# Performance work log

Measured on AMD Instinct MI355X. Metric: run time of the kernel, lower is better.

The kernel has to match this reference:

```python
import jax, jax.numpy as jnp
import numpy as np

B, T, D, H = 2, 2048, 1024, 16
DH = D // H  # 64


def setup_inputs() -> dict:
    key = jax.random.key(0)
    k1, k2, k3 = jax.random.split(key, 3)
    x = jax.random.normal(k1, (B, T, D), dtype=jnp.float32)
    # torch nn.Linear(d, 3d, bias=False): y = x @ W.T; we store W already transposed as [in, out]
    Wqkv = jax.random.normal(k2, (D, 3 * D), dtype=jnp.float32) * (1.0 / np.sqrt(D))
    Wproj = jax.random.normal(k3, (D, D), dtype=jnp.float32) * (1.0 / np.sqrt(D))
    return {"x": x, "Wqkv": Wqkv, "Wproj": Wproj}


def reference(x, Wqkv, Wproj):
    Bx, Tx, C = x.shape
    qkv = x @ Wqkv                                   # [B,T,3C]
    q, k, v = jnp.split(qkv, 3, axis=-1)
    def rs(t):
        return t.reshape(Bx, Tx, H, DH).transpose(0, 2, 1, 3)  # [B,H,T,DH]
    q, k, v = rs(q), rs(k), rs(v)
    scale = 1.0 / jnp.sqrt(jnp.asarray(DH, dtype=x.dtype))
    att = jnp.einsum('bhqd,bhkd->bhqk', q, k) * scale          # [B,H,T,T]
    causal = jnp.tril(jnp.ones((Tx, Tx), dtype=bool))
    att = jnp.where(causal[None, None, :, :], att, jnp.asarray(-jnp.inf, dtype=att.dtype))
    att = jax.nn.softmax(att, axis=-1)
    out = jnp.einsum('bhqk,bhkd->bhqd', att, v)                # [B,H,T,DH]
    out = out.transpose(0, 2, 1, 3).reshape(Bx, Tx, C)         # [B,T,C]
    return out @ Wproj
```

## Files before the change

kernel.cpp:

```cpp
#include <hip/hip_runtime.h>
#include <hip/hip_bf16.h>

#define BB 2
#define TT 2048
#define DD 1024
#define HH 16
#define MM (BB*TT)
#define N3 (3*DD)
#define QKW 2048

typedef __attribute__((ext_vector_type(8))) short short8;
typedef __attribute__((ext_vector_type(4))) float f32x4;
typedef __attribute__((ext_vector_type(16))) float f32x16;

#define ZERO16 (f32x16){0,0,0,0,0,0,0,0,0,0,0,0,0,0,0,0}

#define GLDS16(g, l) __builtin_amdgcn_global_load_lds( \
    (const __attribute__((address_space(1))) void*)(g), \
    (__attribute__((address_space(3))) void*)(l), 16, 0, 0)

__device__ __forceinline__ unsigned short f2bf(float f) {
    union { float f; unsigned u; } v; v.f = f;
    unsigned r = v.u + 0x7FFFu + ((v.u >> 16) & 1u);
    return (unsigned short)(r >> 16);
}

__device__ __forceinline__ unsigned cvt_pk_bf16(float lo, float hi) {
    unsigned r;
    asm("v_cvt_pk_bf16_f32 %0, %1, %2" : "=v"(r) : "v"(lo), "v"(hi));
    return r;
}

__device__ __forceinline__ float fast_exp2(float x) {
    float r;
    asm("v_exp_f32 %0, %1" : "=v"(r) : "v"(x));
    return r;
}
__device__ __forceinline__ float fast_rcp(float x) {
    float r;
    asm("v_rcp_f32 %0, %1" : "=v"(r) : "v"(x));
    return r;
}

__global__ void prep_kernel(const float* __restrict__ x,
                            const float* __restrict__ Wqkv,
                            const float* __restrict__ Wproj,
                            unsigned short* __restrict__ xb,
                            unsigned short* __restrict__ wqkvt,
                            unsigned short* __restrict__ wprojt) {
    __shared__ float tile[32][33];
    const int bid = blockIdx.x;
    const int tx = threadIdx.x, ty = threadIdx.y;
    if (bid < 4096) {
        const float* src;
        unsigned short* dst;
        int rows, cols, c0, r0;
        if (bid < 3072) {
            src = Wqkv; dst = wqkvt; rows = DD; cols = N3;
            c0 = (bid % 96) * 32; r0 = (bid / 96) * 32;
        } else {
            src = Wproj; dst = wprojt; rows = DD; cols = DD;
            int b2 = bid - 3072;
            c0 = (b2 & 31) * 32; r0 = (b2 >> 5) * 32;
        }
#pragma unroll
        for (int i = 0; i < 4; i++) {
            int r = ty + i * 8;
            tile[r][tx] = src[(size_t)(r0 + r) * cols + c0 + tx];
        }
        __syncthreads();
#pragma unroll
        for (int i = 0; i < 4; i++) {
            int r = ty + i * 8;
            dst[(size_t)(c0 + r) * rows + r0 + tx] = f2bf(tile[tx][r]);
        }
    } else {
        const int t = ty * 32 + tx;
        int i = (bid - 4096) * 256 + t;
#pragma unroll
        for (int k = 0; k < 2; k++, i += 262144) {
            const float4* s = reinterpret_cast<const float4*>(x) + (size_t)i * 2;
            float4 a = s[0], b = s[1];
            unsigned short r[8] = {f2bf(a.x), f2bf(a.y), f2bf(a.z), f2bf(a.w),
                                   f2bf(b.x), f2bf(b.y), f2bf(b.z), f2bf(b.w)};
            *reinterpret_cast<uint4*>(xb + (size_t)i * 8) = *reinterpret_cast<uint4*>(r);
        }
    }
}

__global__ __launch_bounds__(512, 2)
void gemm256_qkv(const unsigned short* __restrict__ A,
                 const unsigned short* __restrict__ Bt,
                 unsigned short* __restrict__ qkv2,
                 unsigned short* __restrict__ Vout,
                 float scale) {
    __shared__ unsigned short Al[2][2][128][64];
    __shared__ unsigned short Bl[2][2][128][64];

    const int id = blockIdx.y * 12 + blockIdx.x;
    const int swzid = (id & 7) * 24 + (id >> 3);
    const int tm = (swzid / 12) * 256, tn = (swzid % 12) * 256;
    const int t = threadIdx.x, w = t >> 6, l = t & 63;
    const int wm = w >> 2, wn = w & 3, bh = wn >> 1;
    const int lo = l & 15, hi = l >> 4;
    const int srow = l >> 3;
    const int sg = (l & 7) ^ srow;

    f32x4 acc[8][4];
#pragma unroll
    for (int i = 0; i < 8; i++)
#pragma unroll
        for (int j = 0; j < 4; j++) acc[i][j] = (f32x4){0.f, 0.f, 0.f, 0.f};

    const unsigned short* Abase = A + (size_t)(tm + w * 16 + srow) * 1024 + sg * 8;
    const unsigned short* Bbase = Bt + (size_t)(tn + w * 16 + srow) * 1024 + sg * 8;

#define STG_A(KT, H) { \
    GLDS16(Abase + (size_t)(H) * 128 * 1024 + ((KT) & 15) * 64, &Al[(KT) & 1][H][w * 16][0]); \
    GLDS16(Abase + (size_t)(H) * 128 * 1024 + 8 * 1024 + ((KT) & 15) * 64, &Al[(KT) & 1][H][w * 16 + 8][0]); }
#define STG_B(KT, H) { \
    GLDS16(Bbase + (size_t)(H) * 128 * 1024 + ((KT) & 15) * 64, &Bl[(KT) & 1][H][w * 16][0]); \
    GLDS16(Bbase + (size_t)(H) * 128 * 1024 + 8 * 1024 + ((KT) & 15) * 64, &Bl[(KT) & 1][H][w * 16 + 8][0]); }

#define LOAD_A(AFR, KP, MH) { \
    const char* ab = (const char*)&Al[KP][wm][0][0]; \
    _Pragma("unroll") \
    for (int fi = 0; fi < 4; fi++) \
    _Pragma("unroll") \
    for (int ks = 0; ks < 2; ks++) \
        AFR[fi][ks] = *reinterpret_cast<const short8*>( \
            ab + ((MH) * 64 + fi * 16 + lo) * 128 + (((ks * 4 + hi) ^ (lo & 7)) << 4)); }
#define LOAD_B(BFR, KP, NH) { \
    const char* bb = (const char*)&Bl[KP][bh][0][0]; \
    _Pragma("unroll") \
    for (int fj = 0; fj < 2; fj++) \
    _Pragma("unroll") \
    for (int ks = 0; ks < 2; ks++) \
        BFR[fj][ks] = *reinterpret_cast<const short8*>( \
            bb + ((wn & 1) * 64 + (NH) * 32 + fj * 16 + lo) * 128 + (((ks * 4 + hi) ^ (lo & 7)) << 4)); }

#define MFMA16(MH, NH, AFR, BFR) { \
    _Pragma("unroll") \
    for (int ks = 0; ks < 2; ks++) \
    _Pragma("unroll") \
    for (int fi = 0; fi < 4; fi++) \
    _Pragma("unroll") \
    for (int fj = 0; fj < 2; fj++) \
        acc[(MH) * 4 + fi][(NH) * 2 + fj] = __builtin_amdgcn_mfma_f32_16x16x32_bf16( \
            AFR[fi][ks], BFR[fj][ks], acc[(MH) * 4 + fi][(NH) * 2 + fj], 0, 0, 0); }

#define BAR __builtin_amdgcn_s_barrier()
#define LGKM0 asm volatile("s_waitcnt lgkmcnt(0)")
#define P1 __builtin_amdgcn_s_setprio(1)
#define P0 __builtin_amdgcn_s_setprio(0)

    STG_A(0, 0); STG_A(0, 1); STG_B(0, 0); STG_B(0, 1);
    STG_B(1, 0); STG_B(1, 1);
    asm volatile("s_waitcnt vmcnt(4)");
    BAR;

    for (int i = 0; i < 8; i++) {
        const int kt = 2 * i;
        short8 AF[4][2], BA[2][2], BBf[2][2];
        LOAD_A(AF, 0, 0); LOAD_B(BA, 0, 0);
        STG_A(kt + 1, 0); STG_A(kt + 1, 1);
        BAR; LGKM0; P1; MFMA16(0, 0, AF, BA); P0; BAR;
        LOAD_B(BBf, 0, 1);
        BAR; LGKM0; P1; MFMA16(0, 1, AF, BBf); P0; BAR;
        LOAD_A(AF, 0, 1);
        STG_B(kt + 2, 0); STG_B(kt + 2, 1);
        BAR; LGKM0; P1; MFMA16(1, 1, AF, BBf); P0; BAR;
        STG_A(kt + 2, 0);
        BAR; LGKM0; P1; MFMA16(1, 0, AF, BA); P0;
        asm volatile("s_waitcnt vmcnt(6)");
        BAR;
        LOAD_A(AF, 1, 0); LOAD_B(BA, 1, 0);
        STG_A(kt + 2, 1);
        BAR; LGKM0; P1; MFMA16(0, 0, AF, BA); P0; BAR;
        LOAD_B(BBf, 1, 1);
        BAR; LGKM0; P1; MFMA16(0, 1, AF, BBf); P0; BAR;
        LOAD_A(AF, 1, 1);
        STG_B(kt + 3, 0); STG_B(kt + 3, 1);
        BAR; LGKM0; P1; MFMA16(1, 1, AF, BBf); P0; BAR;
        BAR; LGKM0; P1; MFMA16(1, 0, AF, BA); P0;
        asm volatile("s_waitcnt vmcnt(4)");
        BAR;
    }

#pragma unroll
    for (int i = 0; i < 8; i++)
#pragma unroll
        for (int j = 0; j < 4; j++) {
            const int col = tn + wn * 64 + j * 16 + lo;
            const int row0 = tm + wm * 128 + i * 16 + hi * 4;
            if (col < 2 * DD) {
                float s = (col < DD) ? scale : 1.0f;
#pragma unroll
                for (int r = 0; r < 4; r++)
                    qkv2[(size_t)(row0 + r) * QKW + col] = f2bf(acc[i][j][r] * s);
            } else {
                unsigned short pk[4];
#pragma unroll
                for (int r = 0; r < 4; r++) pk[r] = f2bf(acc[i][j][r]);
                *reinterpret_cast<uint2*>(&Vout[(size_t)(col - 2 * DD) * MM + row0]) =
                    *reinterpret_cast<uint2*>(pk);
            }
        }
#undef STG_A
#undef STG_B
#undef LOAD_A
#undef LOAD_B
#undef MFMA16
#undef BAR
#undef LGKM0
#undef P1
#undef P0
}

__global__ __launch_bounds__(256)
void gemm_proj(const unsigned short* __restrict__ A,
               const unsigned short* __restrict__ Bt,
               float* __restrict__ Cout) {
    __shared__ unsigned short As[128][64];
    __shared__ unsigned short Bs[64][64];
    const int nbx = 16;
    const int id = blockIdx.y * nbx + blockIdx.x;
    const int cpx = 512 >> 3;
    const int swz = (id & 7) * cpx + (id >> 3);
    const int tm = (swz / nbx) * 128, tn = (swz % nbx) * 64;
    const int t = threadIdx.x;
    const int w = t >> 6, lane = t & 63, lo = lane & 15, hi = lane >> 4;
    const int wr = w >> 1, wc = w & 1;

    f32x4 acc[4][2];
#pragma unroll
    for (int i = 0; i < 4; i++)
#pragma unroll
        for (int j = 0; j < 2; j++) acc[i][j] = (f32x4){0.f, 0.f, 0.f, 0.f};

    const int sr8 = lane >> 3;
    const int scol = (lane & 7) * 8;
    const unsigned short* ga = &A[(size_t)(tm + w * 32 + sr8) * 1024 + scol];
    const unsigned short* gb = &Bt[(size_t)(tn + w * 16 + sr8) * 1024 + scol];

    for (int k0 = 0; k0 < 1024; k0 += 64) {
        __syncthreads();
#pragma unroll
        for (int i = 0; i < 4; i++)
            GLDS16(ga + (size_t)(i * 8) * 1024 + k0, &As[w * 32 + i * 8][0]);
#pragma unroll
        for (int i = 0; i < 2; i++)
            GLDS16(gb + (size_t)(i * 8) * 1024 + k0, &Bs[w * 16 + i * 8][0]);
        __syncthreads();

        short8 af[4][2], bf[2][2];
#pragma unroll
        for (int i = 0; i < 4; i++)
#pragma unroll
            for (int ks = 0; ks < 2; ks++)
                af[i][ks] = *reinterpret_cast<const short8*>(&As[wr * 64 + i * 16 + lo][ks * 32 + hi * 8]);
#pragma unroll
        for (int j = 0; j < 2; j++)
#pragma unroll
            for (int ks = 0; ks < 2; ks++)
                bf[j][ks] = *reinterpret_cast<const short8*>(&Bs[wc * 32 + j * 16 + lo][ks * 32 + hi * 8]);
#pragma unroll
        for (int ks = 0; ks < 2; ks++)
#pragma unroll
            for (int i = 0; i < 4; i++)
#pragma unroll
                for (int j = 0; j < 2; j++)
                    acc[i][j] = __builtin_amdgcn_mfma_f32_16x16x32_bf16(af[i][ks], bf[j][ks], acc[i][j], 0, 0, 0);
    }
#pragma unroll
    for (int i = 0; i < 4; i++)
#pragma unroll
        for (int j = 0; j < 2; j++) {
            const int col = tn + wc * 32 + j * 16 + lo;
            const int row0 = tm + wr * 64 + i * 16 + hi * 4;
#pragma unroll
            for (int r = 0; r < 4; r++)
                Cout[(size_t)(row0 + r) * DD + col] = acc[i][j][r];
        }
}

__global__ __launch_bounds__(256)
void attn_kernel(const unsigned short* __restrict__ qkv2,
                 const unsigned short* __restrict__ vtg,
                 unsigned short* __restrict__ outp) {
    __shared__ unsigned short Ks[3][64][64];
    __shared__ unsigned short Vt[3][64][64];

    const int b = blockIdx.z, h = blockIdx.x, p = blockIdx.y;
    const int qcl = p, qch = 31 - p;
    const int L = p + 1, Hn = 32 - p;
    const int t = threadIdx.x;
    const int w = t >> 6, l = t & 63, ql = l & 31, hi8 = l >> 5;
    const int pr = w >> 1, rg = w & 1;
    const int q0h = qch * 64 + rg * 32;
    const int q0p = (pr ? qcl : qch) * 64 + rg * 32;
    const unsigned short* base2 = qkv2 + (size_t)b * TT * QKW;

    short8 bq[4];
#pragma unroll
    for (int ks = 0; ks < 4; ks++)
        bq[ks] = *reinterpret_cast<const short8*>(
            &base2[(size_t)(q0p + ql) * QKW + h * 64 + ks * 16 + hi8 * 8]);

    f32x16 o0 = ZERO16, o1 = ZERO16, lD = ZERO16;

    short8 ones1;
#pragma unroll
    for (int j = 0; j < 8; j++) ones1[j] = (short)0x3F80;

    const int krow = l >> 3;
    const int kc8 = (l & 7) ^ krow;
    const unsigned short* gk = &base2[(size_t)(w * 8 + krow) * QKW + DD + h * 64 + kc8 * 8];
    const unsigned short* gv = &vtg[(size_t)(h * 64 + w * 8 + krow) * MM + b * TT + kc8 * 8];

#define STAGE(KVB, BUF) { \
    GLDS16(gk + (size_t)(KVB) * QKW, &Ks[BUF][w * 8][0]); \
    GLDS16(gk + (size_t)((KVB) + 32) * QKW, &Ks[BUF][32 + w * 8][0]); \
    GLDS16(gv + (KVB), &Vt[BUF][w * 8][0]); \
    GLDS16(gv + (size_t)32 * MM + (KVB), &Vt[BUF][32 + w * 8][0]); }

#define WRITE_OUT(Q0) { \
    _Pragma("unroll") \
    for (int r = 0; r < 16; r++) { \
        int src = (r & 3) + 8 * (r >> 2) + 4 * hi8; \
        float inv = fast_rcp(lD[r]); \
        size_t off = (size_t)(b * TT + (Q0) + src) * DD + h * 64 + ql; \
        outp[off] = f2bf(o0[r] * inv); \
        outp[off + 32] = f2bf(o1[r] * inv); \
    } }

    STAGE(0, 0);
    STAGE(64, 1);
    asm volatile("s_waitcnt vmcnt(4)");
    __builtin_amdgcn_s_barrier();

    const int sw4 = (ql & 7) << 4;
    int cur = 0;
    for (int kvt = 0; kvt < Hn; kvt++) {
        const bool deep = (kvt + 2) < Hn;
        if (deep) { STAGE((kvt + 2) * 64, cur == 0 ? 2 : cur - 1); }

        if (kvt == L && pr == 1) {
            WRITE_OUT(qcl * 64 + rg * 32);
            o0 = ZERO16; o1 = ZERO16; lD = ZERO16;
#pragma unroll
            for (int ks = 0; ks < 4; ks++)
                bq[ks] = *reinterpret_cast<const short8*>(
                    &base2[(size_t)(q0h + ql) * QKW + h * 64 + ks * 16 + hi8 * 8]);
        }

        const char* kbase = (const char*)&Ks[cur][0][0];
        const char* vbase = (const char*)&Vt[cur][0][0];
        const int kvb = kvt * 64;

        if (kvt < L) {
            short8 ak0[4], ak1[4];
#pragma unroll
            for (int ks = 0; ks < 4; ks++) {
                ak0[ks] = *reinterpret_cast<const short8*>(kbase + ql * 128 + (((ks * 2 + hi8) << 4) ^ sw4));
                ak1[ks] = *reinterpret_cast<const short8*>(kbase + (32 + ql) * 128 + (((ks * 2 + hi8) << 4) ^ sw4));
            }
            f32x16 sa0 = ZERO16, sa1 = ZERO16;
#pragma unroll
            for (int ks = 0; ks < 4; ks++) {
                sa0 = __builtin_amdgcn_mfma_f32_32x32x16_bf16(ak0[ks], bq[ks], sa0, 0, 0, 0);
                sa1 = __builtin_amdgcn_mfma_f32_32x32x16_bf16(ak1[ks], bq[ks], sa1, 0, 0, 0);
            }
            if (pr == 1 && kvt == L - 1) {
                const int qg = q0p + ql;
#pragma unroll
                for (int r = 0; r < 16; r++) {
                    int crow = (r & 3) + 8 * (r >> 2) + 4 * hi8;
                    if (kvb + crow > qg) sa0[r] = -1e30f;
                    if (kvb + 32 + crow > qg) sa1[r] = -1e30f;
                }
            }
#pragma unroll
            for (int r = 0; r < 16; r++) sa0[r] = fast_exp2(sa0[r]);
#pragma unroll
            for (int r = 0; r < 16; r++) sa1[r] = fast_exp2(sa1[r]);

            unsigned a01 = cvt_pk_bf16(sa0[0], sa0[1]),  a23 = cvt_pk_bf16(sa0[2], sa0[3]);
            unsigned a45 = cvt_pk_bf16(sa0[4], sa0[5]),  a67 = cvt_pk_bf16(sa0[6], sa0[7]);
            asm("v_permlane32_swap_b32 %0, %1" : "+v"(a01), "+v"(a45));
            asm("v_permlane32_swap_b32 %0, %1" : "+v"(a23), "+v"(a67));
            unsigned b01 = cvt_pk_bf16(sa0[8], sa0[9]),  b23 = cvt_pk_bf16(sa0[10], sa0[11]);
            unsigned b45 = cvt_pk_bf16(sa0[12], sa0[13]), b67 = cvt_pk_bf16(sa0[14], sa0[15]);
            asm("v_permlane32_swap_b32 %0, %1" : "+v"(b01), "+v"(b45));
            asm("v_permlane32_swap_b32 %0, %1" : "+v"(b23), "+v"(b67));
            unsigned c01 = cvt_pk_bf16(sa1[0], sa1[1]),  c23 = cvt_pk_bf16(sa1[2], sa1[3]);
            unsigned c45 = cvt_pk_bf16(sa1[4], sa1[5]),  c67 = cvt_pk_bf16(sa1[6], sa1[7]);
            asm("v_permlane32_swap_b32 %0, %1" : "+v"(c01), "+v"(c45));
            asm("v_permlane32_swap_b32 %0, %1" : "+v"(c23), "+v"(c67));
            unsigned d01 = cvt_pk_bf16(sa1[8], sa1[9]),  d23 = cvt_pk_bf16(sa1[10], sa1[11]);
            unsigned d45 = cvt_pk_bf16(sa1[12], sa1[13]), d67 = cvt_pk_bf16(sa1[14], sa1[15]);
            asm("v_permlane32_swap_b32 %0, %1" : "+v"(d01), "+v"(d45));
            asm("v_permlane32_swap_b32 %0, %1" : "+v"(d23), "+v"(d67));
            union { unsigned u[4]; short8 s; } f0s0, f1s0, f0s1, f1s1;
            f0s0.u[0] = a01; f0s0.u[1] = a23; f0s0.u[2] = a45; f0s0.u[3] = a67;
            f1s0.u[0] = b01; f1s0.u[1] = b23; f1s0.u[2] = b45; f1s0.u[3] = b67;
            f0s1.u[0] = c01; f0s1.u[1] = c23; f0s1.u[2] = c45; f0s1.u[3] = c67;
            f1s1.u[0] = d01; f1s1.u[1] = d23; f1s1.u[2] = d45; f1s1.u[3] = d67;

            lD = __builtin_amdgcn_mfma_f32_32x32x16_bf16(f0s0.s, ones1, lD, 0, 0, 0);
            lD = __builtin_amdgcn_mfma_f32_32x32x16_bf16(f1s0.s, ones1, lD, 0, 0, 0);
            lD = __builtin_amdgcn_mfma_f32_32x32x16_bf16(f0s1.s, ones1, lD, 0, 0, 0);
            lD = __builtin_amdgcn_mfma_f32_32x32x16_bf16(f1s1.s, ones1, lD, 0, 0, 0);

            short8 bv00 = *reinterpret_cast<const short8*>(vbase + ql * 128 + (((0 + hi8) << 4) ^ sw4));
            short8 bv01 = *reinterpret_cast<const short8*>(vbase + ql * 128 + (((2 + hi8) << 4) ^ sw4));
            short8 bv02 = *reinterpret_cast<const short8*>(vbase + ql * 128 + (((4 + hi8) << 4) ^ sw4));
            short8 bv03 = *reinterpret_cast<const short8*>(vbase + ql * 128 + (((6 + hi8) << 4) ^ sw4));
            short8 bv10 = *reinterpret_cast<const short8*>(vbase + (32 + ql) * 128 + (((0 + hi8) << 4) ^ sw4));
            short8 bv11 = *reinterpret_cast<const short8*>(vbase + (32 + ql) * 128 + (((2 + hi8) << 4) ^ sw4));
            short8 bv12 = *reinterpret_cast<const short8*>(vbase + (32 + ql) * 128 + (((4 + hi8) << 4) ^ sw4));
            short8 bv13 = *reinterpret_cast<const short8*>(vbase + (32 + ql) * 128 + (((6 + hi8) << 4) ^ sw4));
            o0 = __builtin_amdgcn_mfma_f32_32x32x16_bf16(f0s0.s, bv00, o0, 0, 0, 0);
            o1 = __builtin_amdgcn_mfma_f32_32x32x16_bf16(f0s0.s, bv10, o1, 0, 0, 0);
            o0 = __builtin_amdgcn_mfma_f32_32x32x16_bf16(f1s0.s, bv01, o0, 0, 0, 0);
            o1 = __builtin_amdgcn_mfma_f32_32x32x16_bf16(f1s0.s, bv11, o1, 0, 0, 0);
            o0 = __builtin_amdgcn_mfma_f32_32x32x16_bf16(f0s1.s, bv02, o0, 0, 0, 0);
            o1 = __builtin_amdgcn_mfma_f32_32x32x16_bf16(f0s1.s, bv12, o1, 0, 0, 0);
            o0 = __builtin_amdgcn_mfma_f32_32x32x16_bf16(f1s1.s, bv03, o0, 0, 0, 0);
            o1 = __builtin_amdgcn_mfma_f32_32x32x16_bf16(f1s1.s, bv13, o1, 0, 0, 0);
        } else {
            const int sub = pr;
            short8 ak[4];
#pragma unroll
            for (int ks = 0; ks < 4; ks++)
                ak[ks] = *reinterpret_cast<const short8*>(
                    kbase + (sub * 32 + ql) * 128 + (((ks * 2 + hi8) << 4) ^ sw4));
            f32x16 sa = ZERO16;
#pragma unroll
            for (int ks = 0; ks < 4; ks++)
                sa = __builtin_amdgcn_mfma_f32_32x32x16_bf16(ak[ks], bq[ks], sa, 0, 0, 0);

            if (kvt == Hn - 1) {
                const int qg = q0h + ql;
#pragma unroll
                for (int r = 0; r < 16; r++) {
                    int crow = (r & 3) + 8 * (r >> 2) + 4 * hi8;
                    if (kvb + sub * 32 + crow > qg) sa[r] = -1e30f;
                }
            }
#pragma unroll
            for (int r = 0; r < 16; r++) sa[r] = fast_exp2(sa[r]);

            unsigned a01 = cvt_pk_bf16(sa[0], sa[1]),  a23 = cvt_pk_bf16(sa[2], sa[3]);
            unsigned a45 = cvt_pk_bf16(sa[4], sa[5]),  a67 = cvt_pk_bf16(sa[6], sa[7]);
            asm("v_permlane32_swap_b32 %0, %1" : "+v"(a01), "+v"(a45));
            asm("v_permlane32_swap_b32 %0, %1" : "+v"(a23), "+v"(a67));
            unsigned b01 = cvt_pk_bf16(sa[8], sa[9]),  b23 = cvt_pk_bf16(sa[10], sa[11]);
            unsigned b45 = cvt_pk_bf16(sa[12], sa[13]), b67 = cvt_pk_bf16(sa[14], sa[15]);
            asm("v_permlane32_swap_b32 %0, %1" : "+v"(b01), "+v"(b45));
            asm("v_permlane32_swap_b32 %0, %1" : "+v"(b23), "+v"(b67));
            union { unsigned u[4]; short8 s; } f0, f1;
            f0.u[0] = a01; f0.u[1] = a23; f0.u[2] = a45; f0.u[3] = a67;
            f1.u[0] = b01; f1.u[1] = b23; f1.u[2] = b45; f1.u[3] = b67;

            lD = __builtin_amdgcn_mfma_f32_32x32x16_bf16(f0.s, ones1, lD, 0, 0, 0);
            lD = __builtin_amdgcn_mfma_f32_32x32x16_bf16(f1.s, ones1, lD, 0, 0, 0);

            short8 bv00 = *reinterpret_cast<const short8*>(vbase + ql * 128 + (((sub * 4 + 0 + hi8) << 4) ^ sw4));
            short8 bv01 = *reinterpret_cast<const short8*>(vbase + ql * 128 + (((sub * 4 + 2 + hi8) << 4) ^ sw4));
            short8 bv10 = *reinterpret_cast<const short8*>(vbase + (32 + ql) * 128 + (((sub * 4 + 0 + hi8) << 4) ^ sw4));
            short8 bv11 = *reinterpret_cast<const short8*>(vbase + (32 + ql) * 128 + (((sub * 4 + 2 + hi8) << 4) ^ sw4));
            o0 = __builtin_amdgcn_mfma_f32_32x32x16_bf16(f0.s, bv00, o0, 0, 0, 0);
            o1 = __builtin_amdgcn_mfma_f32_32x32x16_bf16(f0.s, bv10, o1, 0, 0, 0);
            o0 = __builtin_amdgcn_mfma_f32_32x32x16_bf16(f1.s, bv01, o0, 0, 0, 0);
            o1 = __builtin_amdgcn_mfma_f32_32x32x16_bf16(f1.s, bv11, o1, 0, 0, 0);
        }

        if (deep) asm volatile("s_waitcnt vmcnt(4)");
        else if (kvt + 1 < Hn) asm volatile("s_waitcnt vmcnt(0)");
        __builtin_amdgcn_s_barrier();
        cur = (cur == 2) ? 0 : cur + 1;
    }

    float* xf = (float*)&Ks[0][0][0];
    float* xl = (float*)&Vt[0][0][0];
    const int tid128 = (w & 1) * 64 + l;
    if (pr == 1) {
#pragma unroll
        for (int r = 0; r < 16; r++) {
            xf[r * 128 + tid128] = o0[r];
            xf[(16 + r) * 128 + tid128] = o1[r];
            xl[r * 128 + tid128] = lD[r];
        }
    }
    __syncthreads();
    if (pr == 0) {
#pragma unroll
        for (int r = 0; r < 16; r++) {
            o0[r] += xf[r * 128 + tid128];
            o1[r] += xf[(16 + r) * 128 + tid128];
            lD[r] += xl[r * 128 + tid128];
        }
        WRITE_OUT(q0h);
    }
#undef STAGE
#undef WRITE_OUT
}

extern "C" void kernel_launch(void* const* d_in, const int* in_sizes, int n_in,
                              void* d_out, int out_size, void* d_ws, size_t ws_size,
                              hipStream_t stream) {
    const float* x     = (const float*)d_in[0];
    const float* Wqkv  = (const float*)d_in[1];
    const float* Wproj = (const float*)d_in[2];
    float* out = (float*)d_out;

    unsigned short* xb     = (unsigned short*)d_ws;
    unsigned short* wqkvt  = xb + (size_t)MM * DD;
    unsigned short* wprojt = wqkvt + (size_t)N3 * DD;
    unsigned short* qkv2   = wprojt + (size_t)DD * DD;
    unsigned short* vtg    = qkv2 + (size_t)MM * QKW;
    unsigned short* attout = vtg + (size_t)DD * MM;
    size_t need = ((size_t)MM * DD + (size_t)N3 * DD + (size_t)DD * DD +
                   (size_t)MM * QKW + (size_t)DD * MM + (size_t)MM * DD) * 2;
    if (ws_size < need) return;

    const float sc = 0.125f * 1.44269504088896f;

    prep_kernel<<<5120, dim3(32, 8), 0, stream>>>(x, Wqkv, Wproj, xb, wqkvt, wprojt);

    gemm256_qkv<<<dim3(12, 16), 512, 0, stream>>>(xb, wqkvt, qkv2, vtg, sc);

    attn_kernel<<<dim3(HH, 16, BB), 256, 0, stream>>>(qkv2, vtg, attout);

    gemm_proj<<<dim3(16, 32), 256, 0, stream>>>(attout, wprojt, out);
}
```

Baseline: 117.6 us.

## Split high-chunk KV tiles between warp pairs so each step does full tiles

The attention loop is restructured into a fixed 17-step schedule. After the low query chunk finishes, the two warp pairs work on different whole KV tiles: the pair that handled the low chunk takes odd tiles and the other pair takes even tiles. Before, both pairs split each tile in half. Only the final diagonal tile is still split. The schedule halves the number of barrier-separated iterations for the high chunk and balances work per block, but it uses a 4-slot LDS ring with a variable number of tiles prefetched per step. It also replaces the explicit vmcnt waits with __syncthreads, which may drain all outstanding loads and lose overlap between loading and compute.

```diff
diff --git a/kernel.cpp b/kernel.cpp
--- a/kernel.cpp
+++ b/kernel.cpp
@@ -284,21 +284,146 @@
         }
 }
 
+struct AttnState {
+    f32x16 o0, o1, lD;
+};
+
+__device__ __forceinline__ void attn_full_tile(
+        const char* kbase, const char* vbase, const short8* bq, short8 ones1,
+        AttnState& st, int sw4, int ql, int hi8, bool domask, int kvb, int qg) {
+    short8 ak0[4], ak1[4];
+#pragma unroll
+    for (int ks = 0; ks < 4; ks++) {
+        ak0[ks] = *reinterpret_cast<const short8*>(kbase + ql * 128 + (((ks * 2 + hi8) << 4) ^ sw4));
+        ak1[ks] = *reinterpret_cast<const short8*>(kbase + (32 + ql) * 128 + (((ks * 2 + hi8) << 4) ^ sw4));
+    }
+    f32x16 sa0 = ZERO16, sa1 = ZERO16;
+#pragma unroll
+    for (int ks = 0; ks < 4; ks++) {
+        sa0 = __builtin_amdgcn_mfma_f32_32x32x16_bf16(ak0[ks], bq[ks], sa0, 0, 0, 0);
+        sa1 = __builtin_amdgcn_mfma_f32_32x32x16_bf16(ak1[ks], bq[ks], sa1, 0, 0, 0);
+    }
+    if (domask) {
+#pragma unroll
+        for (int r = 0; r < 16; r++) {
+            int crow = (r & 3) + 8 * (r >> 2) + 4 * hi8;
+            if (kvb + crow > qg) sa0[r] = -1e30f;
+            if (kvb + 32 + crow > qg) sa1[r] = -1e30f;
+        }
+    }
+#pragma unroll
+    for (int r = 0; r < 16; r++) sa0[r] = fast_exp2(sa0[r]);
+#pragma unroll
+    for (int r = 0; r < 16; r++) sa1[r] = fast_exp2(sa1[r]);
+
+    unsigned a01 = cvt_pk_bf16(sa0[0], sa0[1]),  a23 = cvt_pk_bf16(sa0[2], sa0[3]);
+    unsigned a45 = cvt_pk_bf16(sa0[4], sa0[5]),  a67 = cvt_pk_bf16(sa0[6], sa0[7]);
+    asm("v_permlane32_swap_b32 %0, %1" : "+v"(a01), "+v"(a45));
+    asm("v_permlane32_swap_b32 %0, %1" : "+v"(a23), "+v"(a67));
+    unsigned b01 = cvt_pk_bf16(sa0[8], sa0[9]),  b23 = cvt_pk_bf16(sa0[10], sa0[11]);
+    unsigned b45 = cvt_pk_bf16(sa0[12], sa0[13]), b67 = cvt_pk_bf16(sa0[14], sa0[15]);
+    asm("v_permlane32_swap_b32 %0, %1" : "+v"(b01), "+v"(b45));
+    asm("v_permlane32_swap_b32 %0, %1" : "+v"(b23), "+v"(b67));
+    unsigned c01 = cvt_pk_bf16(sa1[0], sa1[1]),  c23 = cvt_pk_bf16(sa1[2], sa1[3]);
+    unsigned c45 = cvt_pk_bf16(sa1[4], sa1[5]),  c67 = cvt_pk_bf16(sa1[6], sa1[7]);
+    asm("v_permlane32_swap_b32 %0, %1" : "+v"(c01), "+v"(c45));
+    asm("v_permlane32_swap_b32 %0, %1" : "+v"(c23), "+v"(c67));
+    unsigned d01 = cvt_pk_bf16(sa1[8], sa1[9]),  d23 = cvt_pk_bf16(sa1[10], sa1[11]);
+    unsigned d45 = cvt_pk_bf16(sa1[12], sa1[13]), d67 = cvt_pk_bf16(sa1[14], sa1[15]);
+    asm("v_permlane32_swap_b32 %0, %1" : "+v"(d01), "+v"(d45));
+    asm("v_permlane32_swap_b32 %0, %1" : "+v"(d23), "+v"(d67));
+    union { unsigned u[4]; short8 s; } f0s0, f1s0, f0s1, f1s1;
+    f0s0.u[0] = a01; f0s0.u[1] = a23; f0s0.u[2] = a45; f0s0.u[3] = a67;
+    f1s0.u[0] = b01; f1s0.u[1] = b23; f1s0.u[2] = b45; f1s0.u[3] = b67;
+    f0s1.u[0] = c01; f0s1.u[1] = c23; f0s1.u[2] = c45; f0s1.u[3] = c67;
+    f1s1.u[0] = d01; f1s1.u[1] = d23; f1s1.u[2] = d45; f1s1.u[3] = d67;
+
+    st.lD = __builtin_amdgcn_mfma_f32_32x32x16_bf16(f0s0.s, ones1, st.lD, 0, 0, 0);
+    st.lD = __builtin_amdgcn_mfma_f32_32x32x16_bf16(f1s0.s, ones1, st.lD, 0, 0, 0);
+    st.lD = __builtin_amdgcn_mfma_f32_32x32x16_bf16(f0s1.s, ones1, st.lD, 0, 0, 0);
+    st.lD = __builtin_amdgcn_mfma_f32_32x32x16_bf16(f1s1.s, ones1, st.lD, 0, 0, 0);
+
+    short8 bv00 = *reinterpret_cast<const short8*>(vbase + ql * 128 + (((0 + hi8) << 4) ^ sw4));
+    short8 bv01 = *reinterpret_cast<const short8*>(vbase + ql * 128 + (((2 + hi8) << 4) ^ sw4));
+    short8 bv02 = *reinterpret_cast<const short8*>(vbase + ql * 128 + (((4 + hi8) << 4) ^ sw4));
+    short8 bv03 = *reinterpret_cast<const short8*>(vbase + ql * 128 + (((6 + hi8) << 4) ^ sw4));
+    short8 bv10 = *reinterpret_cast<const short8*>(vbase + (32 + ql) * 128 + (((0 + hi8) << 4) ^ sw4));
+    short8 bv11 = *reinterpret_cast<const short8*>(vbase + (32 + ql) * 128 + (((2 + hi8) << 4) ^ sw4));
+    short8 bv12 = *reinterpret_cast<const short8*>(vbase + (32 + ql) * 128 + (((4 + hi8) << 4) ^ sw4));
+    short8 bv13 = *reinterpret_cast<const short8*>(vbase + (32 + ql) * 128 + (((6 + hi8) << 4) ^ sw4));
+    st.o0 = __builtin_amdgcn_mfma_f32_32x32x16_bf16(f0s0.s, bv00, st.o0, 0, 0, 0);
+    st.o1 = __builtin_amdgcn_mfma_f32_32x32x16_bf16(f0s0.s, bv10, st.o1, 0, 0, 0);
+    st.o0 = __builtin_amdgcn_mfma_f32_32x32x16_bf16(f1s0.s, bv01, st.o0, 0, 0, 0);
+    st.o1 = __builtin_amdgcn_mfma_f32_32x32x16_bf16(f1s0.s, bv11, st.o1, 0, 0, 0);
+    st.o0 = __builtin_amdgcn_mfma_f32_32x32x16_bf16(f0s1.s, bv02, st.o0, 0, 0, 0);
+    st.o1 = __builtin_amdgcn_mfma_f32_32x32x16_bf16(f0s1.s, bv12, st.o1, 0, 0, 0);
+    st.o0 = __builtin_amdgcn_mfma_f32_32x32x16_bf16(f1s1.s, bv03, st.o0, 0, 0, 0);
+    st.o1 = __builtin_amdgcn_mfma_f32_32x32x16_bf16(f1s1.s, bv13, st.o1, 0, 0, 0);
+}
+
+__device__ __forceinline__ void attn_half_tile(
+        const char* kbase, const char* vbase, const short8* bq, short8 ones1,
+        AttnState& st, int sw4, int ql, int hi8, int sub, int kvb, int qg) {
+    short8 ak[4];
+#pragma unroll
+    for (int ks = 0; ks < 4; ks++)
+        ak[ks] = *reinterpret_cast<const short8*>(
+            kbase + (sub * 32 + ql) * 128 + (((ks * 2 + hi8) << 4) ^ sw4));
+    f32x16 sa = ZERO16;
+#pragma unroll
+    for (int ks = 0; ks < 4; ks++)
+        sa = __builtin_amdgcn_mfma_f32_32x32x16_bf16(ak[ks], bq[ks], sa, 0, 0, 0);
+
+#pragma unroll
+    for (int r = 0; r < 16; r++) {
+        int crow = (r & 3) + 8 * (r >> 2) + 4 * hi8;
+        if (kvb + sub * 32 + crow > qg) sa[r] = -1e30f;
+    }
+#pragma unroll
+    for (int r = 0; r < 16; r++) sa[r] = fast_exp2(sa[r]);
+
+    unsigned a01 = cvt_pk_bf16(sa[0], sa[1]),  a23 = cvt_pk_bf16(sa[2], sa[3]);
+    unsigned a45 = cvt_pk_bf16(sa[4], sa[5]),  a67 = cvt_pk_bf16(sa[6], sa[7]);
+    asm("v_permlane32_swap_b32 %0, %1" : "+v"(a01), "+v"(a45));
+    asm("v_permlane32_swap_b32 %0, %1" : "+v"(a23), "+v"(a67));
+    unsigned b01 = cvt_pk_bf16(sa[8], sa[9]),  b23 = cvt_pk_bf16(sa[10], sa[11]);
+    unsigned b45 = cvt_pk_bf16(sa[12], sa[13]), b67 = cvt_pk_bf16(sa[14], sa[15]);
+    asm("v_permlane32_swap_b32 %0, %1" : "+v"(b01), "+v"(b45));
+    asm("v_permlane32_swap_b32 %0, %1" : "+v"(b23), "+v"(b67));
+    union { unsigned u[4]; short8 s; } f0, f1;
+    f0.u[0] = a01; f0.u[1] = a23; f0.u[2] = a45; f0.u[3] = a67;
+    f1.u[0] = b01; f1.u[1] = b23; f1.u[2] = b45; f1.u[3] = b67;
+
+    st.lD = __builtin_amdgcn_mfma_f32_32x32x16_bf16(f0.s, ones1, st.lD, 0, 0, 0);
+    st.lD = __builtin_amdgcn_mfma_f32_32x32x16_bf16(f1.s, ones1, st.lD, 0, 0, 0);
+
+    short8 bv00 = *reinterpret_cast<const short8*>(vbase + ql * 128 + (((sub * 4 + 0 + hi8) << 4) ^ sw4));
+    short8 bv01 = *reinterpret_cast<const short8*>(vbase + ql * 128 + (((sub * 4 + 2 + hi8) << 4) ^ sw4));
+    short8 bv10 = *reinterpret_cast<const short8*>(vbase + (32 + ql) * 128 + (((sub * 4 + 0 + hi8) << 4) ^ sw4));
+    short8 bv11 = *reinterpret_cast<const short8*>(vbase + (32 + ql) * 128 + (((sub * 4 + 2 + hi8) << 4) ^ sw4));
+    st.o0 = __builtin_amdgcn_mfma_f32_32x32x16_bf16(f0.s, bv00, st.o0, 0, 0, 0);
+    st.o1 = __builtin_amdgcn_mfma_f32_32x32x16_bf16(f0.s, bv10, st.o1, 0, 0, 0);
+    st.o0 = __builtin_amdgcn_mfma_f32_32x32x16_bf16(f1.s, bv01, st.o0, 0, 0, 0);
+    st.o1 = __builtin_amdgcn_mfma_f32_32x32x16_bf16(f1.s, bv11, st.o1, 0, 0, 0);
+}
+
 __global__ __launch_bounds__(256)
 void attn_kernel(const unsigned short* __restrict__ qkv2,
                  const unsigned short* __restrict__ vtg,
                  unsigned short* __restrict__ outp) {
-    __shared__ unsigned short Ks[3][64][64];
-    __shared__ unsigned short Vt[3][64][64];
+    __shared__ unsigned short Ks[4][64][64];
+    __shared__ unsigned short Vt[4][64][64];
 
     const int b = blockIdx.z, h = blockIdx.x, p = blockIdx.y;
     const int qcl = p, qch = 31 - p;
     const int L = p + 1, Hn = 32 - p;
+    const int NSTEP = 17;
     const int t = threadIdx.x;
     const int w = t >> 6, l = t & 63, ql = l & 31, hi8 = l >> 5;
     const int pr = w >> 1, rg = w & 1;
     const int q0h = qch * 64 + rg * 32;
-    const int q0p = (pr ? qcl : qch) * 64 + rg * 32;
+    const int q0l = qcl * 64 + rg * 32;
+    const int q0p = pr ? q0l : q0h;
     const unsigned short* base2 = qkv2 + (size_t)b * TT * QKW;
 
     short8 bq[4];
@@ -307,7 +432,8 @@
         bq[ks] = *reinterpret_cast<const short8*>(
             &base2[(size_t)(q0p + ql) * QKW + h * 64 + ks * 16 + hi8 * 8]);
 
-    f32x16 o0 = ZERO16, o1 = ZERO16, lD = ZERO16;
+    AttnState st;
+    st.o0 = ZERO16; st.o1 = ZERO16; st.lD = ZERO16;
 
     short8 ones1;
 #pragma unroll
@@ -318,168 +444,70 @@
     const unsigned short* gk = &base2[(size_t)(w * 8 + krow) * QKW + DD + h * 64 + kc8 * 8];
     const unsigned short* gv = &vtg[(size_t)(h * 64 + w * 8 + krow) * MM + b * TT + kc8 * 8];
 
-#define STAGE(KVB, BUF) { \
-    GLDS16(gk + (size_t)(KVB) * QKW, &Ks[BUF][w * 8][0]); \
-    GLDS16(gk + (size_t)((KVB) + 32) * QKW, &Ks[BUF][32 + w * 8][0]); \
-    GLDS16(gv + (KVB), &Vt[BUF][w * 8][0]); \
-    GLDS16(gv + (size_t)32 * MM + (KVB), &Vt[BUF][32 + w * 8][0]); }
+#define STAGE(TI) { \
+    const int _s = (TI) & 3; \
+    const size_t _kb = (size_t)(TI) * 64; \
+    GLDS16(gk + _kb * QKW, &Ks[_s][w * 8][0]); \
+    GLDS16(gk + (_kb + 32) * QKW, &Ks[_s][32 + w * 8][0]); \
+    GLDS16(gv + _kb, &Vt[_s][w * 8][0]); \
+    GLDS16(gv + (size_t)32 * MM + _kb, &Vt[_s][32 + w * 8][0]); }
 
 #define WRITE_OUT(Q0) { \
     _Pragma("unroll") \
     for (int r = 0; r < 16; r++) { \
         int src = (r & 3) + 8 * (r >> 2) + 4 * hi8; \
-        float inv = fast_rcp(lD[r]); \
+        float inv = fast_rcp(st.lD[r]); \
         size_t off = (size_t)(b * TT + (Q0) + src) * DD + h * 64 + ql; \
-        outp[off] = f2bf(o0[r] * inv); \
-        outp[off + 32] = f2bf(o1[r] * inv); \
+        outp[off] = f2bf(st.o0[r] * inv); \
+        outp[off + 32] = f2bf(st.o1[r] * inv); \
     } }
 
-    STAGE(0, 0);
-    STAGE(64, 1);
-    asm volatile("s_waitcnt vmcnt(4)");
-    __builtin_amdgcn_s_barrier();
+    STAGE(0);
+    int nIss = 1;
+    __syncthreads();
 
     const int sw4 = (ql & 7) << 4;
-    int cur = 0;
-    for (int kvt = 0; kvt < Hn; kvt++) {
-        const bool deep = (kvt + 2) < Hn;
-        if (deep) { STAGE((kvt + 2) * 64, cur == 0 ? 2 : cur - 1); }
-
-        if (kvt == L && pr == 1) {
-            WRITE_OUT(qcl * 64 + rg * 32);
-            o0 = ZERO16; o1 = ZERO16; lD = ZERO16;
+    for (int s = 0; s < NSTEP; s++) {
+        {
+            const int sn = s + 1;
+            int lastN;
+            if (sn < L) lastN = sn;
+            else if (sn < NSTEP - 1) lastN = L + 2 * (sn - L) + 1;
+            else if (sn == NSTEP - 1) lastN = Hn - 1;
+            else lastN = -1;
+            while (nIss <= lastN) { STAGE(nIss); nIss++; }
+        }
+
+        if (s == L && pr == 1) {
+            WRITE_OUT(q0l);
+            st.o0 = ZERO16; st.o1 = ZERO16; st.lD = ZERO16;
 #pragma unroll
             for (int ks = 0; ks < 4; ks++)
                 bq[ks] = *reinterpret_cast<const short8*>(
                     &base2[(size_t)(q0h + ql) * QKW + h * 64 + ks * 16 + hi8 * 8]);
         }
 
-        const char* kbase = (const char*)&Ks[cur][0][0];
-        const char* vbase = (const char*)&Vt[cur][0][0];
-        const int kvb = kvt * 64;
-
-        if (kvt < L) {
-            short8 ak0[4], ak1[4];
-#pragma unroll
-            for (int ks = 0; ks < 4; ks++) {
-                ak0[ks] = *reinterpret_cast<const short8*>(kbase + ql * 128 + (((ks * 2 + hi8) << 4) ^ sw4));
-                ak1[ks] = *reinterpret_cast<const short8*>(kbase + (32 + ql) * 128 + (((ks * 2 + hi8) << 4) ^ sw4));
-            }
-            f32x16 sa0 = ZERO16, sa1 = ZERO16;
-#pragma unroll
-            for (int ks = 0; ks < 4; ks++) {
-                sa0 = __builtin_amdgcn_mfma_f32_32x32x16_bf16(ak0[ks], bq[ks], sa0, 0, 0, 0);
-                sa1 = __builtin_amdgcn_mfma_f32_32x32x16_bf16(ak1[ks], bq[ks], sa1, 0, 0, 0);
-            }
-            if (pr == 1 && kvt == L - 1) {
-                const int qg = q0p + ql;
-#pragma unroll
-                for (int r = 0; r < 16; r++) {
-                    int crow = (r & 3) + 8 * (r >> 2) + 4 * hi8;
-                    if (kvb + crow > qg) sa0[r] = -1e30f;
-                    if (kvb + 32 + crow > qg) sa1[r] = -1e30f;
-                }
-            }
-#pragma unroll
-            for (int r = 0; r < 16; r++) sa0[r] = fast_exp2(sa0[r]);
-#pragma unroll
-            for (int r = 0; r < 16; r++) sa1[r] = fast_exp2(sa1[r]);
-
-            unsigned a01 = cvt_pk_bf16(sa0[0], sa0[1]),  a23 = cvt_pk_bf16(sa0[2], sa0[3]);
-            unsigned a45 = cvt_pk_bf16(sa0[4], sa0[5]),  a67 = cvt_pk_bf16(sa0[6], sa0[7]);
-            asm("v_permlane32_swap_b32 %0, %1" : "+v"(a01), "+v"(a45));
-            asm("v_permlane32_swap_b32 %0, %1" : "+v"(a23), "+v"(a67));
-            unsigned b01 = cvt_pk_bf16(sa0[8], sa0[9]),  b23 = cvt_pk_bf16(sa0[10], sa0[11]);
-            unsigned b45 = cvt_pk_bf16(sa0[12], sa0[13]), b67 = cvt_pk_bf16(sa0[14], sa0[15]);
-            asm("v_permlane32_swap_b32 %0, %1" : "+v"(b01), "+v"(b45));
-            asm("v_permlane32_swap_b32 %0, %1" : "+v"(b23), "+v"(b67));
-            unsigned c01 = cvt_pk_bf16(sa1[0], sa1[1]),  c23 = cvt_pk_bf16(sa1[2], sa1[3]);
-            unsigned c45 = cvt_pk_bf16(sa1[4], sa1[5]),  c67 = cvt_pk_bf16(sa1[6], sa1[7]);
-            asm("v_permlane32_swap_b32 %0, %1" : "+v"(c01), "+v"(c45));
-            asm("v_permlane32_swap_b32 %0, %1" : "+v"(c23), "+v"(c67));
-            unsigned d01 = cvt_pk_bf16(sa1[8], sa1[9]),  d23 = cvt_pk_bf16(sa1[10], sa1[11]);
-            unsigned d45 = cvt_pk_bf16(sa1[12], sa1[13]), d67 = cvt_pk_bf16(sa1[14], sa1[15]);
-            asm("v_permlane32_swap_b32 %0, %1" : "+v"(d01), "+v"(d45));
-            asm("v_permlane32_swap_b32 %0, %1" : "+v"(d23), "+v"(d67));
-            union { unsigned u[4]; short8 s; } f0s0, f1s0, f0s1, f1s1;
-            f0s0.u[0] = a01; f0s0.u[1] = a23; f0s0.u[2] = a45; f0s0.u[3] = a67;
-            f1s0.u[0] = b01; f1s0.u[1] = b23; f1s0.u[2] = b45; f1s0.u[3] = b67;
-            f0s1.u[0] = c01; f0s1.u[1] = c23; f0s1.u[2] = c45; f0s1.u[3] = c67;
-            f1s1.u[0] = d01; f1s1.u[1] = d23; f1s1.u[2] = d45; f1s1.u[3] = d67;
-
-            lD = __builtin_amdgcn_mfma_f32_32x32x16_bf16(f0s0.s, ones1, lD, 0, 0, 0);
-            lD = __builtin_amdgcn_mfma_f32_32x32x16_bf16(f1s0.s, ones1, lD, 0, 0, 0);
-            lD = __builtin_amdgcn_mfma_f32_32x32x16_bf16(f0s1.s, ones1, lD, 0, 0, 0);
-            lD = __builtin_amdgcn_mfma_f32_32x32x16_bf16(f1s1.s, ones1, lD, 0, 0, 0);
-
-            short8 bv00 = *reinterpret_cast<const short8*>(vbase + ql * 128 + (((0 + hi8) << 4) ^ sw4));
-            short8 bv01 = *reinterpret_cast<const short8*>(vbase + ql * 128 + (((2 + hi8) << 4) ^ sw4));
-            short8 bv02 = *reinterpret_cast<const short8*>(vbase + ql * 128 + (((4 + hi8) << 4) ^ sw4));
-            short8 bv03 = *reinterpret_cast<const short8*>(vbase + ql * 128 + (((6 + hi8) << 4) ^ sw4));
-            short8 bv10 = *reinterpret_cast<const short8*>(vbase + (32 + ql) * 128 + (((0 + hi8) << 4) ^ sw4));
-            short8 bv11 = *reinterpret_cast<const short8*>(vbase + (32 + ql) * 128 + (((2 + hi8) << 4) ^ sw4));
-            short8 bv12 = *reinterpret_cast<const short8*>(vbase + (32 + ql) * 128 + (((4 + hi8) << 4) ^ sw4));
-            short8 bv13 = *reinterpret_cast<const short8*>(vbase + (32 + ql) * 128 + (((6 + hi8) << 4) ^ sw4));
-            o0 = __builtin_amdgcn_mfma_f32_32x32x16_bf16(f0s0.s, bv00, o0, 0, 0, 0);
-            o1 = __builtin_amdgcn_mfma_f32_32x32x16_bf16(f0s0.s, bv10, o1, 0, 0, 0);
-            o0 = __builtin_amdgcn_mfma_f32_32x32x16_bf16(f1s0.s, bv01, o0, 0, 0, 0);
-            o1 = __builtin_amdgcn_mfma_f32_32x32x16_bf16(f1s0.s, bv11, o1, 0, 0, 0);
-            o0 = __builtin_amdgcn_mfma_f32_32x32x16_bf16(f0s1.s, bv02, o0, 0, 0, 0);
-            o1 = __builtin_amdgcn_mfma_f32_32x32x16_bf16(f0s1.s, bv12, o1, 0, 0, 0);
-            o0 = __builtin_amdgcn_mfma_f32_32x32x16_bf16(f1s1.s, bv03, o0, 0, 0, 0);
-            o1 = __builtin_amdgcn_mfma_f32_32x32x16_bf16(f1s1.s, bv13, o1, 0, 0, 0);
+        if (s < L) {
+            const int tile = s;
+            const char* kbase = (const char*)&Ks[tile & 3][0][0];
+            const char* vbase = (const char*)&Vt[tile & 3][0][0];
+            const bool domask = (pr == 1) && (s == L - 1);
+            attn_full_tile(kbase, vbase, bq, ones1, st, sw4, ql, hi8,
+                           domask, tile * 64, q0p + ql);
+        } else if (s < NSTEP - 1) {
+            const int tile = L + 2 * (s - L) + pr;
+            const char* kbase = (const char*)&Ks[tile & 3][0][0];
+            const char* vbase = (const char*)&Vt[tile & 3][0][0];
+            attn_full_tile(kbase, vbase, bq, ones1, st, sw4, ql, hi8,
+                           false, 0, 0);
         } else {
-            const int sub = pr;
-            short8 ak[4];
-#pragma unroll
-            for (int ks = 0; ks < 4; ks++)
-                ak[ks] = *reinterpret_cast<const short8*>(
-                    kbase + (sub * 32 + ql) * 128 + (((ks * 2 + hi8) << 4) ^ sw4));
-            f32x16 sa = ZERO16;
-#pragma unroll
-            for (int ks = 0; ks < 4; ks++)
-                sa = __builtin_amdgcn_mfma_f32_32x32x16_bf16(ak[ks], bq[ks], sa, 0, 0, 0);
-
-            if (kvt == Hn - 1) {
-                const int qg = q0h + ql;
-#pragma unroll
-                for (int r = 0; r < 16; r++) {
-                    int crow = (r & 3) + 8 * (r >> 2) + 4 * hi8;
-                    if (kvb + sub * 32 + crow > qg) sa[r] = -1e30f;
-                }
-            }
-#pragma unroll
-            for (int r = 0; r < 16; r++) sa[r] = fast_exp2(sa[r]);
-
-            unsigned a01 = cvt_pk_bf16(sa[0], sa[1]),  a23 = cvt_pk_bf16(sa[2], sa[3]);
-            unsigned a45 = cvt_pk_bf16(sa[4], sa[5]),  a67 = cvt_pk_bf16(sa[6], sa[7]);
-            asm("v_permlane32_swap_b32 %0, %1" : "+v"(a01), "+v"(a45));
-            asm("v_permlane32_swap_b32 %0, %1" : "+v"(a23), "+v"(a67));
-            unsigned b01 = cvt_pk_bf16(sa[8], sa[9]),  b23 = cvt_pk_bf16(sa[10], sa[11]);
-            unsigned b45 = cvt_pk_bf16(sa[12], sa[13]), b67 = cvt_pk_bf16(sa[14], sa[15]);
-            asm("v_permlane32_swap_b32 %0, %1" : "+v"(b01), "+v"(b45));
-            asm("v_permlane32_swap_b32 %0, %1" : "+v"(b23), "+v"(b67));
-            union { unsigned u[4]; short8 s; } f0, f1;
-            f0.u[0] = a01; f0.u[1] = a23; f0.u[2] = a45; f0.u[3] = a67;
-            f1.u[0] = b01; f1.u[1] = b23; f1.u[2] = b45; f1.u[3] = b67;
-
-            lD = __builtin_amdgcn_mfma_f32_32x32x16_bf16(f0.s, ones1, lD, 0, 0, 0);
-            lD = __builtin_amdgcn_mfma_f32_32x32x16_bf16(f1.s, ones1, lD, 0, 0, 0);
-
-            short8 bv00 = *reinterpret_cast<const short8*>(vbase + ql * 128 + (((sub * 4 + 0 + hi8) << 4) ^ sw4));
-            short8 bv01 = *reinterpret_cast<const short8*>(vbase + ql * 128 + (((sub * 4 + 2 + hi8) << 4) ^ sw4));
-            short8 bv10 = *reinterpret_cast<const short8*>(vbase + (32 + ql) * 128 + (((sub * 4 + 0 + hi8) << 4) ^ sw4));
-            short8 bv11 = *reinterpret_cast<const short8*>(vbase + (32 + ql) * 128 + (((sub * 4 + 2 + hi8) << 4) ^ sw4));
-            o0 = __builtin_amdgcn_mfma_f32_32x32x16_bf16(f0.s, bv00, o0, 0, 0, 0);
-            o1 = __builtin_amdgcn_mfma_f32_32x32x16_bf16(f0.s, bv10, o1, 0, 0, 0);
-            o0 = __builtin_amdgcn_mfma_f32_32x32x16_bf16(f1.s, bv01, o0, 0, 0, 0);
-            o1 = __builtin_amdgcn_mfma_f32_32x32x16_bf16(f1.s, bv11, o1, 0, 0, 0);
-        }
-
-        if (deep) asm volatile("s_waitcnt vmcnt(4)");
-        else if (kvt + 1 < Hn) asm volatile("s_waitcnt vmcnt(0)");
-        __builtin_amdgcn_s_barrier();
-        cur = (cur == 2) ? 0 : cur + 1;
+            const int tile = Hn - 1;
+            const char* kbase = (const char*)&Ks[tile & 3][0][0];
+            const char* vbase = (const char*)&Vt[tile & 3][0][0];
+            attn_half_tile(kbase, vbase, bq, ones1, st, sw4, ql, hi8,
+                           pr, tile * 64, q0h + ql);
+        }
+        __syncthreads();
     }
 
     float* xf = (float*)&Ks[0][0][0];
@@ -488,18 +516,18 @@
     if (pr == 1) {
 #pragma unroll
         for (int r = 0; r < 16; r++) {
-            xf[r * 128 + tid128] = o0[r];
-            xf[(16 + r) * 128 + tid128] = o1[r];
-            xl[r * 128 + tid128] = lD[r];
+            xf[r * 128 + tid128] = st.o0[r];
+            xf[(16 + r) * 128 + tid128] = st.o1[r];
+            xl[r * 128 + tid128] = st.lD[r];
         }
     }
     __syncthreads();
     if (pr == 0) {
 #pragma unroll
         for (int r = 0; r < 16; r++) {
-            o0[r] += xf[r * 128 + tid128];
-            o1[r] += xf[(16 + r) * 128 + tid128];
-            lD[r] += xl[r * 128 + tid128];
+            st.o0[r] += xf[r * 128 + tid128];
+            st.o1[r] += xf[(16 + r) * 128 + tid128];
+            st.lD[r] += xl[r * 128 + tid128];
         }
         WRITE_OUT(q0h);
     }
```

Measured after the change: 110.0 us. 6.5% less time.
